# Performance work log

Measured on AMD Instinct MI355X. Metric: run time of the kernel, lower is better.

## Reference

```python
import jax, jax.numpy as jnp
import numpy as np

ALPHA = 0.2  # LeakyReLU negative slope
NEG_INF = -9e15  # mask value used by the torch dense GAT layer

def _gat_layer(x, adj, W, a1, a2):
    # x: [N, F], W: [F, Fh], a1/a2: [Fh]
    Wh = x @ W                                   # [N, Fh]
    f1 = Wh @ a1                                 # [N] source scores
    f2 = Wh @ a2                                 # [N] dest scores
    e = jax.nn.leaky_relu(f1[:, None] + f2[None, :], ALPHA)  # [N, N]
    att = jnp.where(adj > 0, e, NEG_INF)
    att = jax.nn.softmax(att, axis=1)
    return att @ Wh                              # [N, Fh]

def setup_inputs():
    key = jax.random.key(0)
    ks = jax.random.split(key, 8)
    N, F, H, Fh, C = 6144, 512, 4, 64, 40
    x = jax.random.normal(ks[0], (N, F), jnp.float32)
    # sparse-ish binary adjacency with self loops (dense storage as in the module)
    adj = (jax.random.uniform(ks[1], (N, N)) < 0.005).astype(jnp.float32)
    adj = jnp.maximum(adj, jnp.eye(N, dtype=jnp.float32))
    s = 1.0 / np.sqrt(Fh)
    W = jax.random.normal(ks[2], (H, F, Fh), jnp.float32) * s
    a1 = jax.random.normal(ks[3], (H, Fh), jnp.float32) * s
    a2 = jax.random.normal(ks[4], (H, Fh), jnp.float32) * s
    so = 1.0 / np.sqrt(C)
    Wo = jax.random.normal(ks[5], (H * Fh, C), jnp.float32) * so
    ao1 = jax.random.normal(ks[6], (C,), jnp.float32) * so
    ao2 = jax.random.normal(ks[7], (C,), jnp.float32) * so
    return {"x": x, "adj": adj, "W": W, "a1": a1, "a2": a2,
            "Wo": Wo, "ao1": ao1, "ao2": ao2}

def reference(x, adj, W, a1, a2, Wo, ao1, ao2):
    N = x.shape[0]
    # multi-head layer (concat=True -> ELU applied inside each head)
    heads = jax.vmap(_gat_layer, in_axes=(None, None, 0, 0, 0))(x, adj, W, a1, a2)  # [H, N, Fh]
    h = jax.nn.elu(heads)
    h = jnp.transpose(h, (1, 0, 2)).reshape(N, -1)   # concat heads -> [N, H*Fh]
    # output attention layer (concat=False), then outer ELU from GAT.forward
    out = jax.nn.elu(_gat_layer(h, adj, Wo, ao1, ao2))  # [N, C]
    return jax.nn.log_softmax(out, axis=1)
```

## Files before the change

kernel.cpp:

```cpp
#include <hip/hip_runtime.h>
#include <stdint.h>

#define N_NODES 6144
#define F_IN 512
#define NHEAD 4
#define FH 64
#define HF 256
#define NCLS 40
#define CAP 192
#define LRELU_ALPHA 0.2f

typedef __bf16 bf16x8 __attribute__((ext_vector_type(8)));
typedef float floatx4 __attribute__((ext_vector_type(4)));
typedef uint16_t u16x8 __attribute__((ext_vector_type(8)));

__device__ __forceinline__ float b2f(uint16_t u){
    union { float f; uint32_t i; } x; x.i = ((uint32_t)u) << 16; return x.f;
}
__device__ __forceinline__ uint16_t f2b(float f){
    union { float f; uint32_t i; } x; x.f = f;
    uint32_t r = x.i + 0x7FFFu + ((x.i >> 16) & 1u);
    return (uint16_t)(r >> 16);
}
__device__ __forceinline__ void cvt_split8(const float* __restrict__ s, bf16x8& hv, bf16x8& lv){
    union { u16x8 u; bf16x8 b; } H, L;
    #pragma unroll
    for (int j = 0; j < 8; j++){
        uint16_t hb = f2b(s[j]);
        H.u[j] = hb;
        L.u[j] = f2b(s[j] - b2f(hb));
    }
    hv = H.b; lv = L.b;
}


__global__ void k_csr_prep(const float* __restrict__ adj, const float* __restrict__ W,
                           const float* __restrict__ Wo,
                           int* __restrict__ cnt, int* __restrict__ idxbuf,
                           uint16_t* __restrict__ Wth, uint16_t* __restrict__ Wtl,
                           uint16_t* __restrict__ Woth, uint16_t* __restrict__ Wotl){
    __shared__ int scnt;
    int b = blockIdx.x, t = threadIdx.x;
    if (b < N_NODES){
        int i = b;
        if (t == 0) scnt = 0;
        __syncthreads();
        const float4* row = reinterpret_cast<const float4*>(adj + (size_t)i * N_NODES);
        int* out = idxbuf + (size_t)i * CAP;
        for (int q = t; q < N_NODES / 4; q += 256){
            float4 v = row[q];
            int j0 = q * 4;
            if (v.x != 0.f){ int p = atomicAdd(&scnt, 1); if (p < CAP) out[p] = j0;     }
            if (v.y != 0.f){ int p = atomicAdd(&scnt, 1); if (p < CAP) out[p] = j0 + 1; }
            if (v.z != 0.f){ int p = atomicAdd(&scnt, 1); if (p < CAP) out[p] = j0 + 2; }
            if (v.w != 0.f){ int p = atomicAdd(&scnt, 1); if (p < CAP) out[p] = j0 + 3; }
        }
        __syncthreads();
        if (t == 0) cnt[i] = scnt < CAP ? scnt : CAP;
    } else if (b < N_NODES + 64){
        int T = (b - N_NODES) * 256 + t;
        int c = T >> 6, q8 = T & 63;
        int h = c >> 6, f = c & 63, k0 = q8 * 8;
        int rt = c >> 4, m = c & 15, kc = q8 >> 2, q = q8 & 3;
        size_t off = ((size_t)(rt * 16 + kc) << 9) + (q * 16 + m) * 8;
        #pragma unroll
        for (int j = 0; j < 8; j++){
            float v = W[h * 32768 + (k0 + j) * 64 + f];
            uint16_t hi = f2b(v);
            Wth[off + j] = hi;
            Wtl[off + j] = f2b(v - b2f(hi));
        }
    } else {
        int T = (b - N_NODES - 64) * 256 + t;
        int c = T >> 8, k = T & 255;
        float v = (c < NCLS) ? Wo[k * NCLS + c] : 0.f;
        uint16_t hi = f2b(v);
        Woth[c * HF + k] = hi;
        Wotl[c * HF + k] = f2b(v - b2f(hi));
    }
}

__global__ void k_gemm1(const float* __restrict__ x,
                        const uint16_t* __restrict__ Wth, const uint16_t* __restrict__ Wtl,
                        const float* __restrict__ a1, const float* __restrict__ a2,
                        uint16_t* __restrict__ Wh1b, float* __restrict__ f1,
                        float* __restrict__ f2){
    __shared__ float sred[2][2][64];
    int w = threadIdx.x >> 6, l = threadIdx.x & 63;
    int h = blockIdx.y, bx = blockIdx.x;
    int m = l & 15, q = l >> 4;
    int rt0 = bx * 4 + (w & 1) * 2;
    int ctl = (w >> 1) * 2;
    const float* pa0 = x + (size_t)(rt0 * 16 + m) * F_IN + q * 8;
    const float* pa1 = pa0 + 16 * F_IN;
    const uint16_t* pb0h = Wth + ((size_t)(h * 4 + ctl) << 13) + l * 8;
    const uint16_t* pb0l = Wtl + ((size_t)(h * 4 + ctl) << 13) + l * 8;
    const uint16_t* pb1h = pb0h + 8192;
    const uint16_t* pb1l = pb0l + 8192;
    floatx4 acc[2][2] = {};
    for (int kc = 0; kc < 16; kc++){
        float av0[8], av1[8];
        *reinterpret_cast<float4*>(av0)     = *reinterpret_cast<const float4*>(pa0 + kc * 32);
        *reinterpret_cast<float4*>(av0 + 4) = *reinterpret_cast<const float4*>(pa0 + kc * 32 + 4);
        *reinterpret_cast<float4*>(av1)     = *reinterpret_cast<const float4*>(pa1 + kc * 32);
        *reinterpret_cast<float4*>(av1 + 4) = *reinterpret_cast<const float4*>(pa1 + kc * 32 + 4);
        bf16x8 b0h = *reinterpret_cast<const bf16x8*>(pb0h + kc * 512);
        bf16x8 b0l = *reinterpret_cast<const bf16x8*>(pb0l + kc * 512);
        bf16x8 b1h = *reinterpret_cast<const bf16x8*>(pb1h + kc * 512);
        bf16x8 b1l = *reinterpret_cast<const bf16x8*>(pb1l + kc * 512);
        bf16x8 a0h, a0l, a1h_, a1l_;
        cvt_split8(av0, a0h, a0l);
        cvt_split8(av1, a1h_, a1l_);
        acc[0][0] = __builtin_amdgcn_mfma_f32_16x16x32_bf16(a0h, b0l, acc[0][0], 0, 0, 0);
        acc[0][0] = __builtin_amdgcn_mfma_f32_16x16x32_bf16(a0l, b0h, acc[0][0], 0, 0, 0);
        acc[0][0] = __builtin_amdgcn_mfma_f32_16x16x32_bf16(a0h, b0h, acc[0][0], 0, 0, 0);
        acc[0][1] = __builtin_amdgcn_mfma_f32_16x16x32_bf16(a0h, b1l, acc[0][1], 0, 0, 0);
        acc[0][1] = __builtin_amdgcn_mfma_f32_16x16x32_bf16(a0l, b1h, acc[0][1], 0, 0, 0);
        acc[0][1] = __builtin_amdgcn_mfma_f32_16x16x32_bf16(a0h, b1h, acc[0][1], 0, 0, 0);
        acc[1][0] = __builtin_amdgcn_mfma_f32_16x16x32_bf16(a1h_, b0l, acc[1][0], 0, 0, 0);
        acc[1][0] = __builtin_amdgcn_mfma_f32_16x16x32_bf16(a1l_, b0h, acc[1][0], 0, 0, 0);
        acc[1][0] = __builtin_amdgcn_mfma_f32_16x16x32_bf16(a1h_, b0h, acc[1][0], 0, 0, 0);
        acc[1][1] = __builtin_amdgcn_mfma_f32_16x16x32_bf16(a1h_, b1l, acc[1][1], 0, 0, 0);
        acc[1][1] = __builtin_amdgcn_mfma_f32_16x16x32_bf16(a1l_, b1h, acc[1][1], 0, 0, 0);
        acc[1][1] = __builtin_amdgcn_mfma_f32_16x16x32_bf16(a1h_, b1h, acc[1][1], 0, 0, 0);
    }
    #pragma unroll
    for (int fr = 0; fr < 2; fr++){
        #pragma unroll
        for (int fc = 0; fc < 2; fc++){
            int col = h * 64 + (ctl + fc) * 16 + m;
            int rowb = (rt0 + fr) * 16 + q * 4;
            #pragma unroll
            for (int r = 0; r < 4; r++)
                Wh1b[(size_t)(rowb + r) * HF + col] = f2b(acc[fr][fc][r]);
        }
    }
    float a1v0 = a1[h * FH + (ctl + 0) * 16 + m];
    float a1v1 = a1[h * FH + (ctl + 1) * 16 + m];
    float a2v0 = a2[h * FH + (ctl + 0) * 16 + m];
    float a2v1 = a2[h * FH + (ctl + 1) * 16 + m];
    #pragma unroll
    for (int fr = 0; fr < 2; fr++){
        #pragma unroll
        for (int r = 0; r < 4; r++){
            float s1 = acc[fr][0][r] * a1v0 + acc[fr][1][r] * a1v1;
            float s2 = acc[fr][0][r] * a2v0 + acc[fr][1][r] * a2v1;
            #pragma unroll
            for (int off = 1; off < 16; off <<= 1){
                s1 += __shfl_xor(s1, off);
                s2 += __shfl_xor(s2, off);
            }
            if (m == 0){
                int lr = ((w & 1) * 2 + fr) * 16 + q * 4 + r;
                sred[w >> 1][0][lr] = s1;
                sred[w >> 1][1][lr] = s2;
            }
        }
    }
    __syncthreads();
    if (threadIdx.x < 64){
        int n = bx * 64 + threadIdx.x;
        f1[h * N_NODES + n] = sred[0][0][threadIdx.x] + sred[1][0][threadIdx.x];
        f2[h * N_NODES + n] = sred[0][1][threadIdx.x] + sred[1][1][threadIdx.x];
    }
}

__global__ void k_attn1(const int* __restrict__ cnt, const int* __restrict__ idxbuf,
                        const uint16_t* __restrict__ Wh1b, const float* __restrict__ f1,
                        const float* __restrict__ f2,
                        uint16_t* __restrict__ hch, uint16_t* __restrict__ hcl){
    int i = blockIdx.x, h = threadIdx.x >> 6, l = threadIdx.x & 63;
    int c = cnt[i];
    __shared__ int   sidx[CAP];
    __shared__ float sp[NHEAD][CAP];
    const int* src = idxbuf + (size_t)i * CAP;
    for (int e = threadIdx.x; e < c; e += 256) sidx[e] = src[e];
    __syncthreads();
    float f1i = f1[h * N_NODES + i];
    const float* f2h = f2 + h * N_NODES;
    float mx = -1e30f;
    for (int e = l; e < c; e += 64){
        float s = f1i + f2h[sidx[e]];
        s = s > 0.f ? s : LRELU_ALPHA * s;
        sp[h][e] = s;
        mx = fmaxf(mx, s);
    }
    for (int off = 32; off; off >>= 1) mx = fmaxf(mx, __shfl_xor(mx, off));
    float ssum = 0.f;
    for (int e = l; e < c; e += 64){
        float p = __expf(sp[h][e] - mx);
        sp[h][e] = p;
        ssum += p;
    }
    for (int off = 32; off; off >>= 1) ssum += __shfl_xor(ssum, off);
    float inv = 1.f / ssum;
    float acc = 0.f;
    const uint16_t* whb = Wh1b + h * FH + l;
    int e = 0;
    for (; e + 4 <= c; e += 4){
        int j0 = sidx[e], j1 = sidx[e+1], j2 = sidx[e+2], j3 = sidx[e+3];
        float v0 = b2f(whb[(size_t)j0 * HF]);
        float v1 = b2f(whb[(size_t)j1 * HF]);
        float v2 = b2f(whb[(size_t)j2 * HF]);
        float v3 = b2f(whb[(size_t)j3 * HF]);
        acc += sp[h][e]*v0 + sp[h][e+1]*v1 + sp[h][e+2]*v2 + sp[h][e+3]*v3;
    }
    for (; e < c; e++)
        acc += sp[h][e] * b2f(whb[(size_t)sidx[e] * HF]);
    acc *= inv;
    float v = acc > 0.f ? acc : __expf(acc) - 1.f;
    uint16_t hi = f2b(v);
    uint16_t lo = f2b(v - b2f(hi));
    size_t o = (size_t)i * HF + h * FH + l;
    hch[o] = hi;
    hcl[o] = lo;
}

__global__ void k_gemm2(const uint16_t* __restrict__ hch, const uint16_t* __restrict__ hcl,
                        const uint16_t* __restrict__ Woth, const uint16_t* __restrict__ Wotl,
                        float* __restrict__ Wh2){
    int w = threadIdx.x >> 6, l = threadIdx.x & 63;
    int r0 = blockIdx.x * 32 + w * 16;
    int c0 = blockIdx.y * 16;
    int m = l & 15, q = l >> 4;
    const uint16_t* pah = hch  + (size_t)(r0 + m) * HF + q * 8;
    const uint16_t* pal = hcl  + (size_t)(r0 + m) * HF + q * 8;
    const uint16_t* pbh = Woth + (size_t)(c0 + m) * HF + q * 8;
    const uint16_t* pbl = Wotl + (size_t)(c0 + m) * HF + q * 8;
    floatx4 acc = {};
    for (int k0 = 0; k0 < HF; k0 += 32){
        bf16x8 ah = *reinterpret_cast<const bf16x8*>(pah + k0);
        bf16x8 al = *reinterpret_cast<const bf16x8*>(pal + k0);
        bf16x8 bh = *reinterpret_cast<const bf16x8*>(pbh + k0);
        bf16x8 bl = *reinterpret_cast<const bf16x8*>(pbl + k0);
        acc = __builtin_amdgcn_mfma_f32_16x16x32_bf16(ah, bl, acc, 0, 0, 0);
        acc = __builtin_amdgcn_mfma_f32_16x16x32_bf16(al, bh, acc, 0, 0, 0);
        acc = __builtin_amdgcn_mfma_f32_16x16x32_bf16(ah, bh, acc, 0, 0, 0);
    }
    int col = c0 + m;
    if (col < NCLS){
        int rowb = r0 + q * 4;
        #pragma unroll
        for (int r = 0; r < 4; r++)
            Wh2[(size_t)(rowb + r) * NCLS + col] = acc[r];
    }
}

__global__ void k_f12o(const float* __restrict__ Wh2, const float* __restrict__ ao1,
                       const float* __restrict__ ao2, float* __restrict__ f1o,
                       float* __restrict__ f2o){
    int w = threadIdx.x >> 6, l = threadIdx.x & 63;
    int n = blockIdx.x * 4 + w;
    float t1 = 0.f, t2 = 0.f;
    if (l < NCLS){
        float v = Wh2[(size_t)n * NCLS + l];
        t1 = v * ao1[l];
        t2 = v * ao2[l];
    }
    for (int off = 32; off; off >>= 1){
        t1 += __shfl_xor(t1, off);
        t2 += __shfl_xor(t2, off);
    }
    if (l == 0){ f1o[n] = t1; f2o[n] = t2; }
}

__global__ void k_attn2(const int* __restrict__ cnt, const int* __restrict__ idxbuf,
                        const float* __restrict__ Wh2, const float* __restrict__ f1o,
                        const float* __restrict__ f2o, float* __restrict__ out){
    int i = blockIdx.x, l = threadIdx.x;
    int c = cnt[i];
    __shared__ int   sidx[CAP];
    __shared__ float sp[CAP];
    const int* src = idxbuf + (size_t)i * CAP;
    for (int e = l; e < c; e += 64) sidx[e] = src[e];
    __syncthreads();
    float f1i = f1o[i];
    float mx = -1e30f;
    for (int e = l; e < c; e += 64){
        float s = f1i + f2o[sidx[e]];
        s = s > 0.f ? s : LRELU_ALPHA * s;
        sp[e] = s;
        mx = fmaxf(mx, s);
    }
    for (int off = 32; off; off >>= 1) mx = fmaxf(mx, __shfl_xor(mx, off));
    __syncthreads();
    float ssum = 0.f;
    for (int e = l; e < c; e += 64){
        float p = __expf(sp[e] - mx);
        sp[e] = p;
        ssum += p;
    }
    for (int off = 32; off; off >>= 1) ssum += __shfl_xor(ssum, off);
    float inv = 1.f / ssum;
    __syncthreads();
    float acc = 0.f;
    if (l < NCLS){
        const float* wb = Wh2 + l;
        int e = 0;
        for (; e + 4 <= c; e += 4){
            int j0 = sidx[e], j1 = sidx[e+1], j2 = sidx[e+2], j3 = sidx[e+3];
            float v0 = wb[(size_t)j0 * NCLS];
            float v1 = wb[(size_t)j1 * NCLS];
            float v2 = wb[(size_t)j2 * NCLS];
            float v3 = wb[(size_t)j3 * NCLS];
            acc += sp[e]*v0 + sp[e+1]*v1 + sp[e+2]*v2 + sp[e+3]*v3;
        }
        for (; e < c; e++)
            acc += sp[e] * wb[(size_t)sidx[e] * NCLS];
        acc *= inv;
    }
    float o = (l < NCLS) ? (acc > 0.f ? acc : __expf(acc) - 1.f) : -1e30f;
    float m2 = o;
    for (int off = 32; off; off >>= 1) m2 = fmaxf(m2, __shfl_xor(m2, off));
    float ex = (l < NCLS) ? __expf(o - m2) : 0.f;
    for (int off = 32; off; off >>= 1) ex += __shfl_xor(ex, off);
    float res = o - m2 - logf(ex);
    if (l < NCLS) out[(size_t)i * NCLS + l] = res;
}

extern "C" void kernel_launch(void* const* d_in, const int* in_sizes, int n_in,
                              void* d_out, int out_size, void* d_ws, size_t ws_size,
                              hipStream_t stream) {
    const float* x   = (const float*)d_in[0];
    const float* adj = (const float*)d_in[1];
    const float* W   = (const float*)d_in[2];
    const float* a1  = (const float*)d_in[3];
    const float* a2  = (const float*)d_in[4];
    const float* Wo  = (const float*)d_in[5];
    const float* ao1 = (const float*)d_in[6];
    const float* ao2 = (const float*)d_in[7];
    float* out = (float*)d_out;

    char* ws = (char*)d_ws;
    int*      nbr_cnt = (int*)     (ws + 0);
    int*      nbr_idx = (int*)     (ws + 24576);
    uint16_t* Wth     = (uint16_t*)(ws + 4743168);
    uint16_t* Wtl     = (uint16_t*)(ws + 5005312);
    uint16_t* Woth    = (uint16_t*)(ws + 5267456);
    uint16_t* Wotl    = (uint16_t*)(ws + 5292032);
    uint16_t* Wh1b    = (uint16_t*)(ws + 5316608);
    float*    f1      = (float*)   (ws + 8462336);
    float*    f2      = (float*)   (ws + 8560640);
    uint16_t* hch     = (uint16_t*)(ws + 8658944);
    uint16_t* hcl     = (uint16_t*)(ws + 11804672);
    float*    Wh2     = (float*)   (ws + 14950400);
    float*    f1o     = (float*)   (ws + 15933440);
    float*    f2o     = (float*)   (ws + 15958016);

    hipLaunchKernelGGL(k_csr_prep, dim3(6256),   dim3(256), 0, stream, adj, W, Wo,
                       nbr_cnt, nbr_idx, Wth, Wtl, Woth, Wotl);
    hipLaunchKernelGGL(k_gemm1,    dim3(96, 4),  dim3(256), 0, stream, x, Wth, Wtl,
                       a1, a2, Wh1b, f1, f2);
    hipLaunchKernelGGL(k_attn1,    dim3(6144),   dim3(256), 0, stream, nbr_cnt, nbr_idx,
                       Wh1b, f1, f2, hch, hcl);
    hipLaunchKernelGGL(k_gemm2,    dim3(192, 3), dim3(128), 0, stream, hch, hcl, Woth, Wotl, Wh2);
    hipLaunchKernelGGL(k_f12o,     dim3(1536),   dim3(256), 0, stream, Wh2, ao1, ao2, f1o, f2o);
    hipLaunchKernelGGL(k_attn2,    dim3(6144),   dim3(64),  0, stream, nbr_cnt, nbr_idx,
                       Wh2, f1o, f2o, out);
}
```

Baseline: 287.7 us.

## Fuse GEMM1 into CSR prep kernel and fold output scores into GEMM2

Merges the CSR-building kernel, the weight preprocessing and the first GEMM into one launch. The GEMM now reads fp32 W directly and splits it to bf16 hi/lo in registers instead of using a pre-transposed buffer. The output-layer score dot products move into the GEMM2 epilogue via atomics, which removes the separate k_f12o kernel, with one block zeroing the accumulators. This cuts two launches and one dependency stage, and lets the GEMM run alongside the adjacency scan. In exchange, W is read with strided scalar loads, extra conversion work is added, and atomic float sums make the results order-nondeterministic.

```diff
diff --git a/kernel.cpp b/kernel.cpp
--- a/kernel.cpp
+++ b/kernel.cpp
@@ -33,16 +33,107 @@
     hv = H.b; lv = L.b;
 }
 
-
-__global__ void k_csr_prep(const float* __restrict__ adj, const float* __restrict__ W,
-                           const float* __restrict__ Wo,
-                           int* __restrict__ cnt, int* __restrict__ idxbuf,
-                           uint16_t* __restrict__ Wth, uint16_t* __restrict__ Wtl,
-                           uint16_t* __restrict__ Woth, uint16_t* __restrict__ Wotl){
-    __shared__ int scnt;
+__global__ void k_A(const float* __restrict__ adj, const float* __restrict__ x,
+                    const float* __restrict__ W, const float* __restrict__ Wo,
+                    const float* __restrict__ a1, const float* __restrict__ a2,
+                    int* __restrict__ cnt, int* __restrict__ idxbuf,
+                    uint16_t* __restrict__ Woth, uint16_t* __restrict__ Wotl,
+                    uint16_t* __restrict__ Wh1b, float* __restrict__ f1,
+                    float* __restrict__ f2, float* __restrict__ f1o,
+                    float* __restrict__ f2o){
     int b = blockIdx.x, t = threadIdx.x;
-    if (b < N_NODES){
-        int i = b;
+    if (b < 384){
+        __shared__ float sred[2][2][64];
+        int w = t >> 6, l = t & 63;
+        int bx = b >> 2, h = b & 3;
+        int m = l & 15, q = l >> 4;
+        int rt0 = bx * 4 + (w & 1) * 2;
+        int ctl = (w >> 1) * 2;
+        const float* pa0 = x + (size_t)(rt0 * 16 + m) * F_IN + q * 8;
+        const float* pa1 = pa0 + 16 * F_IN;
+        const float* pb = W + h * 32768 + q * 8 * 64 + ctl * 16 + m;
+        floatx4 acc[2][2] = {};
+        for (int kc = 0; kc < 16; kc++){
+            float av0[8], av1[8], bv0[8], bv1[8];
+            *reinterpret_cast<float4*>(av0)     = *reinterpret_cast<const float4*>(pa0 + kc * 32);
+            *reinterpret_cast<float4*>(av0 + 4) = *reinterpret_cast<const float4*>(pa0 + kc * 32 + 4);
+            *reinterpret_cast<float4*>(av1)     = *reinterpret_cast<const float4*>(pa1 + kc * 32);
+            *reinterpret_cast<float4*>(av1 + 4) = *reinterpret_cast<const float4*>(pa1 + kc * 32 + 4);
+            const float* pbk = pb + kc * 2048;
+            #pragma unroll
+            for (int j = 0; j < 8; j++){
+                bv0[j] = pbk[j * 64];
+                bv1[j] = pbk[j * 64 + 16];
+            }
+            bf16x8 a0h, a0l, a1h_, a1l_, b0h, b0l, b1h, b1l;
+            cvt_split8(av0, a0h, a0l);
+            cvt_split8(av1, a1h_, a1l_);
+            cvt_split8(bv0, b0h, b0l);
+            cvt_split8(bv1, b1h, b1l);
+            acc[0][0] = __builtin_amdgcn_mfma_f32_16x16x32_bf16(a0h, b0l, acc[0][0], 0, 0, 0);
+            acc[0][0] = __builtin_amdgcn_mfma_f32_16x16x32_bf16(a0l, b0h, acc[0][0], 0, 0, 0);
+            acc[0][0] = __builtin_amdgcn_mfma_f32_16x16x32_bf16(a0h, b0h, acc[0][0], 0, 0, 0);
+            acc[0][1] = __builtin_amdgcn_mfma_f32_16x16x32_bf16(a0h, b1l, acc[0][1], 0, 0, 0);
+            acc[0][1] = __builtin_amdgcn_mfma_f32_16x16x32_bf16(a0l, b1h, acc[0][1], 0, 0, 0);
+            acc[0][1] = __builtin_amdgcn_mfma_f32_16x16x32_bf16(a0h, b1h, acc[0][1], 0, 0, 0);
+            acc[1][0] = __builtin_amdgcn_mfma_f32_16x16x32_bf16(a1h_, b0l, acc[1][0], 0, 0, 0);
+            acc[1][0] = __builtin_amdgcn_mfma_f32_16x16x32_bf16(a1l_, b0h, acc[1][0], 0, 0, 0);
+            acc[1][0] = __builtin_amdgcn_mfma_f32_16x16x32_bf16(a1h_, b0h, acc[1][0], 0, 0, 0);
+            acc[1][1] = __builtin_amdgcn_mfma_f32_16x16x32_bf16(a1h_, b1l, acc[1][1], 0, 0, 0);
+            acc[1][1] = __builtin_amdgcn_mfma_f32_16x16x32_bf16(a1l_, b1h, acc[1][1], 0, 0, 0);
+            acc[1][1] = __builtin_amdgcn_mfma_f32_16x16x32_bf16(a1h_, b1h, acc[1][1], 0, 0, 0);
+        }
+        #pragma unroll
+        for (int fr = 0; fr < 2; fr++){
+            #pragma unroll
+            for (int fc = 0; fc < 2; fc++){
+                int col = h * 64 + (ctl + fc) * 16 + m;
+                int rowb = (rt0 + fr) * 16 + q * 4;
+                #pragma unroll
+                for (int r = 0; r < 4; r++)
+                    Wh1b[(size_t)(rowb + r) * HF + col] = f2b(acc[fr][fc][r]);
+            }
+        }
+        float a1v0 = a1[h * FH + (ctl + 0) * 16 + m];
+        float a1v1 = a1[h * FH + (ctl + 1) * 16 + m];
+        float a2v0 = a2[h * FH + (ctl + 0) * 16 + m];
+        float a2v1 = a2[h * FH + (ctl + 1) * 16 + m];
+        #pragma unroll
+        for (int fr = 0; fr < 2; fr++){
+            #pragma unroll
+            for (int r = 0; r < 4; r++){
+                float s1 = acc[fr][0][r] * a1v0 + acc[fr][1][r] * a1v1;
+                float s2 = acc[fr][0][r] * a2v0 + acc[fr][1][r] * a2v1;
+                #pragma unroll
+                for (int off = 1; off < 16; off <<= 1){
+                    s1 += __shfl_xor(s1, off);
+                    s2 += __shfl_xor(s2, off);
+                }
+                if (m == 0){
+                    int lr = ((w & 1) * 2 + fr) * 16 + q * 4 + r;
+                    sred[w >> 1][0][lr] = s1;
+                    sred[w >> 1][1][lr] = s2;
+                }
+            }
+        }
+        __syncthreads();
+        if (t < 64){
+            int n = bx * 64 + t;
+            f1[h * N_NODES + n] = sred[0][0][t] + sred[1][0][t];
+            f2[h * N_NODES + n] = sred[0][1][t] + sred[1][1][t];
+        }
+    } else if (b < 432){
+        int T = (b - 384) * 256 + t;
+        int c = T >> 8, k = T & 255;
+        float v = (c < NCLS) ? Wo[k * NCLS + c] : 0.f;
+        uint16_t hi = f2b(v);
+        Woth[c * HF + k] = hi;
+        Wotl[c * HF + k] = f2b(v - b2f(hi));
+    } else if (b == 432){
+        for (int i = t; i < N_NODES; i += 256){ f1o[i] = 0.f; f2o[i] = 0.f; }
+    } else {
+        __shared__ int scnt;
+        int i = b - 433;
         if (t == 0) scnt = 0;
         __syncthreads();
         const float4* row = reinterpret_cast<const float4*>(adj + (size_t)i * N_NODES);
@@ -57,111 +148,6 @@
         }
         __syncthreads();
         if (t == 0) cnt[i] = scnt < CAP ? scnt : CAP;
-    } else if (b < N_NODES + 64){
-        int T = (b - N_NODES) * 256 + t;
-        int c = T >> 6, q8 = T & 63;
-        int h = c >> 6, f = c & 63, k0 = q8 * 8;
-        int rt = c >> 4, m = c & 15, kc = q8 >> 2, q = q8 & 3;
-        size_t off = ((size_t)(rt * 16 + kc) << 9) + (q * 16 + m) * 8;
-        #pragma unroll
-        for (int j = 0; j < 8; j++){
-            float v = W[h * 32768 + (k0 + j) * 64 + f];
-            uint16_t hi = f2b(v);
-            Wth[off + j] = hi;
-            Wtl[off + j] = f2b(v - b2f(hi));
-        }
-    } else {
-        int T = (b - N_NODES - 64) * 256 + t;
-        int c = T >> 8, k = T & 255;
-        float v = (c < NCLS) ? Wo[k * NCLS + c] : 0.f;
-        uint16_t hi = f2b(v);
-        Woth[c * HF + k] = hi;
-        Wotl[c * HF + k] = f2b(v - b2f(hi));
-    }
-}
-
-__global__ void k_gemm1(const float* __restrict__ x,
-                        const uint16_t* __restrict__ Wth, const uint16_t* __restrict__ Wtl,
-                        const float* __restrict__ a1, const float* __restrict__ a2,
-                        uint16_t* __restrict__ Wh1b, float* __restrict__ f1,
-                        float* __restrict__ f2){
-    __shared__ float sred[2][2][64];
-    int w = threadIdx.x >> 6, l = threadIdx.x & 63;
-    int h = blockIdx.y, bx = blockIdx.x;
-    int m = l & 15, q = l >> 4;
-    int rt0 = bx * 4 + (w & 1) * 2;
-    int ctl = (w >> 1) * 2;
-    const float* pa0 = x + (size_t)(rt0 * 16 + m) * F_IN + q * 8;
-    const float* pa1 = pa0 + 16 * F_IN;
-    const uint16_t* pb0h = Wth + ((size_t)(h * 4 + ctl) << 13) + l * 8;
-    const uint16_t* pb0l = Wtl + ((size_t)(h * 4 + ctl) << 13) + l * 8;
-    const uint16_t* pb1h = pb0h + 8192;
-    const uint16_t* pb1l = pb0l + 8192;
-    floatx4 acc[2][2] = {};
-    for (int kc = 0; kc < 16; kc++){
-        float av0[8], av1[8];
-        *reinterpret_cast<float4*>(av0)     = *reinterpret_cast<const float4*>(pa0 + kc * 32);
-        *reinterpret_cast<float4*>(av0 + 4) = *reinterpret_cast<const float4*>(pa0 + kc * 32 + 4);
-        *reinterpret_cast<float4*>(av1)     = *reinterpret_cast<const float4*>(pa1 + kc * 32);
-        *reinterpret_cast<float4*>(av1 + 4) = *reinterpret_cast<const float4*>(pa1 + kc * 32 + 4);
-        bf16x8 b0h = *reinterpret_cast<const bf16x8*>(pb0h + kc * 512);
-        bf16x8 b0l = *reinterpret_cast<const bf16x8*>(pb0l + kc * 512);
-        bf16x8 b1h = *reinterpret_cast<const bf16x8*>(pb1h + kc * 512);
-        bf16x8 b1l = *reinterpret_cast<const bf16x8*>(pb1l + kc * 512);
-        bf16x8 a0h, a0l, a1h_, a1l_;
-        cvt_split8(av0, a0h, a0l);
-        cvt_split8(av1, a1h_, a1l_);
-        acc[0][0] = __builtin_amdgcn_mfma_f32_16x16x32_bf16(a0h, b0l, acc[0][0], 0, 0, 0);
-        acc[0][0] = __builtin_amdgcn_mfma_f32_16x16x32_bf16(a0l, b0h, acc[0][0], 0, 0, 0);
-        acc[0][0] = __builtin_amdgcn_mfma_f32_16x16x32_bf16(a0h, b0h, acc[0][0], 0, 0, 0);
-        acc[0][1] = __builtin_amdgcn_mfma_f32_16x16x32_bf16(a0h, b1l, acc[0][1], 0, 0, 0);
-        acc[0][1] = __builtin_amdgcn_mfma_f32_16x16x32_bf16(a0l, b1h, acc[0][1], 0, 0, 0);
-        acc[0][1] = __builtin_amdgcn_mfma_f32_16x16x32_bf16(a0h, b1h, acc[0][1], 0, 0, 0);
-        acc[1][0] = __builtin_amdgcn_mfma_f32_16x16x32_bf16(a1h_, b0l, acc[1][0], 0, 0, 0);
-        acc[1][0] = __builtin_amdgcn_mfma_f32_16x16x32_bf16(a1l_, b0h, acc[1][0], 0, 0, 0);
-        acc[1][0] = __builtin_amdgcn_mfma_f32_16x16x32_bf16(a1h_, b0h, acc[1][0], 0, 0, 0);
-        acc[1][1] = __builtin_amdgcn_mfma_f32_16x16x32_bf16(a1h_, b1l, acc[1][1], 0, 0, 0);
-        acc[1][1] = __builtin_amdgcn_mfma_f32_16x16x32_bf16(a1l_, b1h, acc[1][1], 0, 0, 0);
-        acc[1][1] = __builtin_amdgcn_mfma_f32_16x16x32_bf16(a1h_, b1h, acc[1][1], 0, 0, 0);
-    }
-    #pragma unroll
-    for (int fr = 0; fr < 2; fr++){
-        #pragma unroll
-        for (int fc = 0; fc < 2; fc++){
-            int col = h * 64 + (ctl + fc) * 16 + m;
-            int rowb = (rt0 + fr) * 16 + q * 4;
-            #pragma unroll
-            for (int r = 0; r < 4; r++)
-                Wh1b[(size_t)(rowb + r) * HF + col] = f2b(acc[fr][fc][r]);
-        }
-    }
-    float a1v0 = a1[h * FH + (ctl + 0) * 16 + m];
-    float a1v1 = a1[h * FH + (ctl + 1) * 16 + m];
-    float a2v0 = a2[h * FH + (ctl + 0) * 16 + m];
-    float a2v1 = a2[h * FH + (ctl + 1) * 16 + m];
-    #pragma unroll
-    for (int fr = 0; fr < 2; fr++){
-        #pragma unroll
-        for (int r = 0; r < 4; r++){
-            float s1 = acc[fr][0][r] * a1v0 + acc[fr][1][r] * a1v1;
-            float s2 = acc[fr][0][r] * a2v0 + acc[fr][1][r] * a2v1;
-            #pragma unroll
-            for (int off = 1; off < 16; off <<= 1){
-                s1 += __shfl_xor(s1, off);
-                s2 += __shfl_xor(s2, off);
-            }
-            if (m == 0){
-                int lr = ((w & 1) * 2 + fr) * 16 + q * 4 + r;
-                sred[w >> 1][0][lr] = s1;
-                sred[w >> 1][1][lr] = s2;
-            }
-        }
-    }
-    __syncthreads();
-    if (threadIdx.x < 64){
-        int n = bx * 64 + threadIdx.x;
-        f1[h * N_NODES + n] = sred[0][0][threadIdx.x] + sred[1][0][threadIdx.x];
-        f2[h * N_NODES + n] = sred[0][1][threadIdx.x] + sred[1][1][threadIdx.x];
     }
 }
 
@@ -218,7 +204,9 @@
 
 __global__ void k_gemm2(const uint16_t* __restrict__ hch, const uint16_t* __restrict__ hcl,
                         const uint16_t* __restrict__ Woth, const uint16_t* __restrict__ Wotl,
-                        float* __restrict__ Wh2){
+                        const float* __restrict__ ao1, const float* __restrict__ ao2,
+                        float* __restrict__ Wh2, float* __restrict__ f1o,
+                        float* __restrict__ f2o){
     int w = threadIdx.x >> 6, l = threadIdx.x & 63;
     int r0 = blockIdx.x * 32 + w * 16;
     int c0 = blockIdx.y * 16;
@@ -238,30 +226,29 @@
         acc = __builtin_amdgcn_mfma_f32_16x16x32_bf16(ah, bh, acc, 0, 0, 0);
     }
     int col = c0 + m;
-    if (col < NCLS){
+    bool valid = col < NCLS;
+    if (valid){
         int rowb = r0 + q * 4;
         #pragma unroll
         for (int r = 0; r < 4; r++)
             Wh2[(size_t)(rowb + r) * NCLS + col] = acc[r];
     }
-}
-
-__global__ void k_f12o(const float* __restrict__ Wh2, const float* __restrict__ ao1,
-                       const float* __restrict__ ao2, float* __restrict__ f1o,
-                       float* __restrict__ f2o){
-    int w = threadIdx.x >> 6, l = threadIdx.x & 63;
-    int n = blockIdx.x * 4 + w;
-    float t1 = 0.f, t2 = 0.f;
-    if (l < NCLS){
-        float v = Wh2[(size_t)n * NCLS + l];
-        t1 = v * ao1[l];
-        t2 = v * ao2[l];
-    }
-    for (int off = 32; off; off >>= 1){
-        t1 += __shfl_xor(t1, off);
-        t2 += __shfl_xor(t2, off);
-    }
-    if (l == 0){ f1o[n] = t1; f2o[n] = t2; }
+    float w1 = valid ? ao1[col] : 0.f;
+    float w2 = valid ? ao2[col] : 0.f;
+    #pragma unroll
+    for (int r = 0; r < 4; r++){
+        float s1 = acc[r] * w1;
+        float s2 = acc[r] * w2;
+        #pragma unroll
+        for (int off = 1; off < 16; off <<= 1){
+            s1 += __shfl_xor(s1, off);
+            s2 += __shfl_xor(s2, off);
+        }
+        if (m == 0){
+            atomicAdd(f1o + r0 + q * 4 + r, s1);
+            atomicAdd(f2o + r0 + q * 4 + r, s2);
+        }
+    }
 }
 
 __global__ void k_attn2(const int* __restrict__ cnt, const int* __restrict__ idxbuf,
@@ -334,27 +321,23 @@
     char* ws = (char*)d_ws;
     int*      nbr_cnt = (int*)     (ws + 0);
     int*      nbr_idx = (int*)     (ws + 24576);
-    uint16_t* Wth     = (uint16_t*)(ws + 4743168);
-    uint16_t* Wtl     = (uint16_t*)(ws + 5005312);
-    uint16_t* Woth    = (uint16_t*)(ws + 5267456);
-    uint16_t* Wotl    = (uint16_t*)(ws + 5292032);
-    uint16_t* Wh1b    = (uint16_t*)(ws + 5316608);
-    float*    f1      = (float*)   (ws + 8462336);
-    float*    f2      = (float*)   (ws + 8560640);
-    uint16_t* hch     = (uint16_t*)(ws + 8658944);
-    uint16_t* hcl     = (uint16_t*)(ws + 11804672);
-    float*    Wh2     = (float*)   (ws + 14950400);
-    float*    f1o     = (float*)   (ws + 15933440);
-    float*    f2o     = (float*)   (ws + 15958016);
-
-    hipLaunchKernelGGL(k_csr_prep, dim3(6256),   dim3(256), 0, stream, adj, W, Wo,
-                       nbr_cnt, nbr_idx, Wth, Wtl, Woth, Wotl);
-    hipLaunchKernelGGL(k_gemm1,    dim3(96, 4),  dim3(256), 0, stream, x, Wth, Wtl,
-                       a1, a2, Wh1b, f1, f2);
-    hipLaunchKernelGGL(k_attn1,    dim3(6144),   dim3(256), 0, stream, nbr_cnt, nbr_idx,
+    uint16_t* Woth    = (uint16_t*)(ws + 4743168);
+    uint16_t* Wotl    = (uint16_t*)(ws + 4767744);
+    uint16_t* Wh1b    = (uint16_t*)(ws + 4792320);
+    float*    f1      = (float*)   (ws + 7938048);
+    float*    f2      = (float*)   (ws + 8036352);
+    uint16_t* hch     = (uint16_t*)(ws + 8134656);
+    uint16_t* hcl     = (uint16_t*)(ws + 11280384);
+    float*    Wh2     = (float*)   (ws + 14426112);
+    float*    f1o     = (float*)   (ws + 15409152);
+    float*    f2o     = (float*)   (ws + 15433728);
+
+    hipLaunchKernelGGL(k_A,     dim3(6577),   dim3(256), 0, stream, adj, x, W, Wo, a1, a2,
+                       nbr_cnt, nbr_idx, Woth, Wotl, Wh1b, f1, f2, f1o, f2o);
+    hipLaunchKernelGGL(k_attn1, dim3(6144),   dim3(256), 0, stream, nbr_cnt, nbr_idx,
                        Wh1b, f1, f2, hch, hcl);
-    hipLaunchKernelGGL(k_gemm2,    dim3(192, 3), dim3(128), 0, stream, hch, hcl, Woth, Wotl, Wh2);
-    hipLaunchKernelGGL(k_f12o,     dim3(1536),   dim3(256), 0, stream, Wh2, ao1, ao2, f1o, f2o);
-    hipLaunchKernelGGL(k_attn2,    dim3(6144),   dim3(64),  0, stream, nbr_cnt, nbr_idx,
+    hipLaunchKernelGGL(k_gemm2, dim3(192, 3), dim3(128), 0, stream, hch, hcl, Woth, Wotl,
+                       ao1, ao2, Wh2, f1o, f2o);
+    hipLaunchKernelGGL(k_attn2, dim3(6144),   dim3(64),  0, stream, nbr_cnt, nbr_idx,
                        Wh2, f1o, f2o, out);
 }
```

Result: faster. 268.8 us (-6.6%).
